# Performance work log

Measured on AMD Instinct MI355X. Metric: run time of the kernel, lower is better.

The kernel has to match this reference:

```python
import jax, jax.numpy as jnp
import numpy as np

K = 20  # n_neighbors
SLOPE = 0.2

def _act(h):
    return jax.nn.leaky_relu(h, negative_slope=SLOPE)

def _knn_indices(pts):
    # pts: (B, 3, N). Returns (B, N, K) indices of nearest neighbors (by -||xi-xj||^2).
    sq = jnp.sum(pts * pts, axis=1)                      # (B, N)
    inner = jnp.einsum('bcn,bcm->bnm', pts, pts)         # (B, N, N)
    neg_dist = 2.0 * inner - sq[:, :, None] - sq[:, None, :]
    _, idx = jax.lax.top_k(neg_dist, K)                  # (B, N, K)
    return idx

def _gather_neighbors(feats, idx):
    # feats: (B, N, C), idx: (B, N, K) -> (B, N, K, C)
    return jax.vmap(lambda f, i: f[i])(feats, idx)

def setup_inputs() -> dict:
    key = jax.random.key(0)
    ks = jax.random.split(key, 7)
    B, N = 16, 2048
    dims = [64, 64, 128, 256]
    s = 0.05
    inp = {
        'x':  jax.random.normal(ks[0], (B, N, 3), jnp.float32),
        'W0': jax.random.normal(ks[1], (dims[0], 6), jnp.float32) * s,
        'b0': jnp.zeros((dims[0],), jnp.float32),
        'W1': jax.random.normal(ks[2], (dims[1], dims[0]), jnp.float32) * s,
        'b1': jnp.zeros((dims[1],), jnp.float32),
        'W2': jax.random.normal(ks[3], (dims[2], dims[1]), jnp.float32) * s,
        'b2': jnp.zeros((dims[2],), jnp.float32),
        'W3': jax.random.normal(ks[4], (dims[3], dims[2]), jnp.float32) * s,
        'b3': jnp.zeros((dims[3],), jnp.float32),
        'Wf': jax.random.normal(ks[5], (1024, sum(dims)), jnp.float32) * s,
        'bf': jnp.zeros((1024,), jnp.float32),
    }
    return inp

def reference(x, W0, b0, W1, b1, W2, b2, W3, b3, Wf, bf):
    # x: (B, N, 3)
    pts = jnp.swapaxes(x, 1, 2)                          # (B, 3, N)
    idx = _knn_indices(pts)                              # (B, N, K)

    # get_graph_features: edge feats = [neighbor - center, center], (B, N, K, 6)
    neigh = _gather_neighbors(x, idx)                    # (B, N, K, 3)
    center = jnp.broadcast_to(x[:, :, None, :], neigh.shape)
    edge = jnp.concatenate([neigh - center, center], axis=-1)

    # EdgeConv (1x1 conv) + act, then max over neighbors
    h = _act(jnp.einsum('bnkc,oc->bnko', edge, W0) + b0)  # (B, N, K, 64)
    feat = jnp.max(h, axis=2)                             # (B, N, 64)

    xs = [feat]
    for W, b in ((W1, b1), (W2, b2), (W3, b3)):
        # graph max pooling over the fixed kNN graph
        pooled = jnp.max(_gather_neighbors(feat, idx), axis=2)  # (B, N, C)
        feat = _act(jnp.einsum('bnc,oc->bno', pooled, W) + b)
        xs.append(feat)

    cat = jnp.concatenate(xs, axis=-1)                    # (B, N, 512)
    out = _act(jnp.einsum('bnc,oc->bno', cat, Wf) + bf)   # (B, N, 1024)
    return jnp.max(out, axis=1)                           # (B, 1024)
```

## Files before the change

kernel.cpp:

```cpp
#include <hip/hip_runtime.h>

#define K_NN 20
#define NEG_INF (-__builtin_inff())

constexpr int BB   = 16;
constexpr int NN   = 2048;
constexpr int CATC = 512;
constexpr int ROW_G = BB * NN;

typedef short bf16x8 __attribute__((ext_vector_type(8)));
typedef float f32x4  __attribute__((ext_vector_type(4)));

__device__ __forceinline__ unsigned short f2bf_rn(float f) {
  unsigned int u = __float_as_uint(f);
  unsigned int r = u + 0x7FFFu + ((u >> 16) & 1u);
  return (unsigned short)(r >> 16);
}
__device__ __forceinline__ float bf2f(unsigned short h) {
  return __uint_as_float((unsigned int)h << 16);
}
__device__ __forceinline__ void split_store(float v, unsigned short* ph, unsigned short* pl) {
  const unsigned short h = f2bf_rn(v);
  *ph = h;
  *pl = f2bf_rn(v - bf2f(h));
}
__device__ __forceinline__ float join_hl(unsigned short h, unsigned short l) {
  return bf2f(h) + bf2f(l);
}

__device__ __forceinline__ int mbcnt(unsigned long long mask) {
  return __builtin_amdgcn_mbcnt_hi((unsigned int)(mask >> 32),
         __builtin_amdgcn_mbcnt_lo((unsigned int)mask, 0));
}

#define DECL_VALS(INIT) \
  unsigned int v0=INIT,v1=INIT,v2=INIT,v3=INIT,v4=INIT,v5=INIT,v6=INIT,v7=INIT, \
               v8=INIT,v9=INIT,v10=INIT,v11=INIT,v12=INIT,v13=INIT,v14=INIT,    \
               v15=INIT,v16=INIT,v17=INIT,v18=INIT,v19=INIT;

#define INSERT_VAL(x) do {                         \
    v19 = min(v18, max(v19, (x)));                 \
    v18 = min(v17, max(v18, (x)));                 \
    v17 = min(v16, max(v17, (x)));                 \
    v16 = min(v15, max(v16, (x)));                 \
    v15 = min(v14, max(v15, (x)));                 \
    v14 = min(v13, max(v14, (x)));                 \
    v13 = min(v12, max(v13, (x)));                 \
    v12 = min(v11, max(v12, (x)));                 \
    v11 = min(v10, max(v11, (x)));                 \
    v10 = min(v9,  max(v10, (x)));                 \
    v9  = min(v8,  max(v9,  (x)));                 \
    v8  = min(v7,  max(v8,  (x)));                 \
    v7  = min(v6,  max(v7,  (x)));                 \
    v6  = min(v5,  max(v6,  (x)));                 \
    v5  = min(v4,  max(v5,  (x)));                 \
    v4  = min(v3,  max(v4,  (x)));                 \
    v3  = min(v2,  max(v3,  (x)));                 \
    v2  = min(v1,  max(v2,  (x)));                 \
    v1  = min(v0,  max(v1,  (x)));                 \
    v0  = max(v0, (x));                            \
  } while (0)

__device__ __forceinline__ unsigned int sortable(float d) {
  unsigned int ub = __float_as_uint(d);
  return (ub & 0x80000000u) ? ~ub : (ub | 0x80000000u);
}

__global__ __launch_bounds__(128) void knn_chunk_kernel(const float* __restrict__ x,
                                                        unsigned int* __restrict__ cv) {
  __shared__ float4 cand[256];
  const int bid = blockIdx.x;
  const int ch = bid & 7;
  const int rt = (bid >> 3) & 15;
  const int b  = bid >> 7;
  const float* xb = x + (size_t)b * NN * 3;

  for (int i = threadIdx.x; i < 256; i += 128) {
    const int m = ch * 256 + i;
    const float px = xb[m*3+0], py = xb[m*3+1], pz = xb[m*3+2];
    cand[i] = make_float4(px, py, pz, fmaf(pz, pz, fmaf(py, py, px*px)));
  }
  __syncthreads();

  const int n = rt * 128 + threadIdx.x;
  const float cx = xb[n*3+0], cy = xb[n*3+1], cz = xb[n*3+2];
  const float csq = fmaf(cz, cz, fmaf(cy, cy, cx*cx));

  DECL_VALS(0u)

#pragma unroll 4
  for (int i = 0; i < 256; ++i) {
    const float4 c = cand[i];
    const float inner = fmaf(cz, c.z, fmaf(cy, c.y, cx*c.x));
    const float d = 2.0f * inner - csq - c.w;
    const unsigned int u = sortable(d);
    INSERT_VAL(u);
  }

  const int rowg = b * NN + n;
#define STORE_VAL(i) cv[(size_t)(ch*K_NN + i) * ROW_G + rowg] = v##i;
  STORE_VAL(0) STORE_VAL(1) STORE_VAL(2) STORE_VAL(3) STORE_VAL(4)
  STORE_VAL(5) STORE_VAL(6) STORE_VAL(7) STORE_VAL(8) STORE_VAL(9)
  STORE_VAL(10) STORE_VAL(11) STORE_VAL(12) STORE_VAL(13) STORE_VAL(14)
  STORE_VAL(15) STORE_VAL(16) STORE_VAL(17) STORE_VAL(18) STORE_VAL(19)
#undef STORE_VAL
}

__global__ __launch_bounds__(64) void knn_d20_kernel(const unsigned int* __restrict__ cv,
                                                     unsigned int* __restrict__ d20g) {
  const int r = blockIdx.x * 64 + threadIdx.x;
#define LOAD_VAL(i) unsigned int v##i = cv[(size_t)i * ROW_G + r];
  LOAD_VAL(0) LOAD_VAL(1) LOAD_VAL(2) LOAD_VAL(3) LOAD_VAL(4)
  LOAD_VAL(5) LOAD_VAL(6) LOAD_VAL(7) LOAD_VAL(8) LOAD_VAL(9)
  LOAD_VAL(10) LOAD_VAL(11) LOAD_VAL(12) LOAD_VAL(13) LOAD_VAL(14)
  LOAD_VAL(15) LOAD_VAL(16) LOAD_VAL(17) LOAD_VAL(18) LOAD_VAL(19)
#undef LOAD_VAL
#pragma unroll 4
  for (int i = K_NN; i < 8 * K_NN; ++i)
    INSERT_VAL(cv[(size_t)i * ROW_G + r]);
  d20g[r] = v19;
}

__global__ __launch_bounds__(256) void knn_collect_kernel(const float* __restrict__ x,
    const unsigned int* __restrict__ d20g, int* __restrict__ idx_out) {
  __shared__ float4 cand[NN];
  __shared__ int tie[4][K_NN];
  const int w = threadIdx.x >> 6, lane = threadIdx.x & 63;
  const int r = blockIdx.x * 4 + w;
  const int b = r >> 11;
  const float* xb = x + (size_t)b * NN * 3;

  for (int i = threadIdx.x; i < NN; i += 256) {
    const float px = xb[i*3+0], py = xb[i*3+1], pz = xb[i*3+2];
    cand[i] = make_float4(px, py, pz, fmaf(pz, pz, fmaf(py, py, px*px)));
  }
  __syncthreads();

  const int n = r & (NN - 1);
  const float4 ctr = cand[n];
  const unsigned int d20 = d20g[r];
  int* op = idx_out + (size_t)r * K_NN;
  int cg = 0, ce = 0;

#pragma unroll 4
  for (int k = 0; k < NN / 64; ++k) {
    const int i = k * 64 + lane;
    const float4 c = cand[i];
    const float inner = fmaf(ctr.z, c.z, fmaf(ctr.y, c.y, ctr.x*c.x));
    const float d = 2.0f * inner - ctr.w - c.w;
    const unsigned int u = sortable(d);
    const unsigned long long mb = __ballot(u > d20);
    if (u > d20) op[cg + mbcnt(mb)] = i;
    cg += __popcll(mb);
    const unsigned long long tb = __ballot(u == d20);
    if (tb) {
      if (u == d20) {
        const int pos = ce + mbcnt(tb);
        if (pos < K_NN) tie[w][pos] = i;
      }
      ce += __popcll(tb);
    }
  }
  if (lane == 0)
    for (int j = 0; cg < K_NN; ++j, ++cg) op[cg] = tie[w][j];
}

__global__ __launch_bounds__(256) void edgeconv_kernel(const float* __restrict__ x,
    const int* __restrict__ idx, const float* __restrict__ W0,
    const float* __restrict__ b0, unsigned short* __restrict__ Ahg,
    unsigned short* __restrict__ Alg) {
  const int o  = threadIdx.x & 63;
  const int pt = blockIdx.x * 4 + (threadIdx.x >> 6);
  const int b  = pt >> 11, n = pt & (NN - 1);
  const float* xb = x + (size_t)b * NN * 3;

  const float w0 = W0[o*6+0], w1 = W0[o*6+1], w2 = W0[o*6+2];
  const float w3 = W0[o*6+3], w4 = W0[o*6+4], w5 = W0[o*6+5];
  const float bias = b0[o];
  const float cx = xb[n*3+0], cy = xb[n*3+1], cz = xb[n*3+2];

  const int* ip = idx + (size_t)pt * K_NN;
  float px = 0.f, py = 0.f, pz = 0.f;
  if (o < K_NN) { const int m = ip[o]; px = xb[m*3+0]; py = xb[m*3+1]; pz = xb[m*3+2]; }

  float best = NEG_INF;
#pragma unroll
  for (int k = 0; k < K_NN; ++k) {
    const float ax = __shfl(px, k, 64), ay = __shfl(py, k, 64), az = __shfl(pz, k, 64);
    float h = w0 * (ax - cx);
    h = fmaf(w1, ay - cy, h);
    h = fmaf(w2, az - cz, h);
    h = fmaf(w3, cx, h);
    h = fmaf(w4, cy, h);
    h = fmaf(w5, cz, h);
    h += bias;
    h = (h > 0.f) ? h : 0.2f * h;
    best = fmaxf(best, h);
  }
  split_store(best, &Ahg[(size_t)pt * CATC + o], &Alg[(size_t)pt * CATC + o]);
}

template<int CIN, int COUT, int PTS>
__global__ __launch_bounds__(256) void pool_mlp_kernel(
    unsigned short* __restrict__ Ahg, unsigned short* __restrict__ Alg,
    const int* __restrict__ idx, const float* __restrict__ W,
    const float* __restrict__ bias, int coff_in, int coff_out) {
  __shared__ float pooled[PTS][CIN];
  __shared__ int sidx[PTS][K_NN];
  const int pt0 = blockIdx.x * PTS;

  for (int t = threadIdx.x; t < PTS * K_NN; t += 256)
    sidx[t / K_NN][t % K_NN] = idx[(size_t)pt0 * K_NN + t];
  __syncthreads();

  for (int t = threadIdx.x; t < PTS * CIN; t += 256) {
    const int p = t / CIN, c = t % CIN;
    const int bq = (pt0 + p) >> 11;
    const size_t base = (size_t)bq * NN * CATC + coff_in + c;
    float mv = NEG_INF;
#pragma unroll
    for (int k = 0; k < K_NN; ++k) {
      const size_t a = base + (size_t)sidx[p][k] * CATC;
      mv = fmaxf(mv, join_hl(Ahg[a], Alg[a]));
    }
    pooled[p][c] = mv;
  }
  __syncthreads();

  for (int t = threadIdx.x; t < PTS * COUT; t += 256) {
    const int p = t / COUT, o = t % COUT;
    const float4* pp = (const float4*)&pooled[p][0];
    const float4* wp = (const float4*)(W + (size_t)o * CIN);
    float acc = 0.f;
#pragma unroll
    for (int c4 = 0; c4 < CIN / 4; ++c4) {
      const float4 pv = pp[c4], wv = wp[c4];
      acc = fmaf(pv.x, wv.x, acc);
      acc = fmaf(pv.y, wv.y, acc);
      acc = fmaf(pv.z, wv.z, acc);
      acc = fmaf(pv.w, wv.w, acc);
    }
    float h = acc + bias[o];
    h = (h > 0.f) ? h : 0.2f * h;
    const size_t a = (size_t)(pt0 + p) * CATC + coff_out + o;
    split_store(h, &Ahg[a], &Alg[a]);
  }
}

__global__ __launch_bounds__(256) void wsplit_kernel(const float* __restrict__ Wf,
    unsigned short* __restrict__ Wh, unsigned short* __restrict__ Wl) {
  const int t = blockIdx.x * 256 + threadIdx.x;
  const float4 v = ((const float4*)Wf)[t];
  ushort4 h4, l4;
  h4.x = f2bf_rn(v.x); l4.x = f2bf_rn(v.x - bf2f(h4.x));
  h4.y = f2bf_rn(v.y); l4.y = f2bf_rn(v.y - bf2f(h4.y));
  h4.z = f2bf_rn(v.z); l4.z = f2bf_rn(v.z - bf2f(h4.z));
  h4.w = f2bf_rn(v.w); l4.w = f2bf_rn(v.w - bf2f(h4.w));
  ((ushort4*)Wh)[t] = h4;
  ((ushort4*)Wl)[t] = l4;
}

__global__ __launch_bounds__(256) void final_gemm_mfma(
    const unsigned short* __restrict__ Ahg, const unsigned short* __restrict__ Alg,
    const unsigned short* __restrict__ Whg, const unsigned short* __restrict__ Wlg,
    float* __restrict__ partials) {
  __shared__ __align__(16) unsigned short AhL[128][40];
  __shared__ __align__(16) unsigned short AlL[128][40];
  __shared__ __align__(16) unsigned short WhL[128][40];
  __shared__ __align__(16) unsigned short WlL[128][40];

  const int L     = blockIdx.x + (blockIdx.y << 3) + (blockIdx.z << 7);
  const int xcd   = L & 7;
  const int q     = L >> 3;
  const int ot    = q & 7;
  const int s     = q >> 3;
  const int p     = (s << 3) | xcd;
  const int chunk = p & 15;
  const int b     = p >> 4;

  const int tid   = threadIdx.x;
  const int lane  = tid & 63;
  const int w     = tid >> 6;
  const int wr    = w >> 1;
  const int wc    = w & 1;
  const int fr    = lane & 15;
  const int kg    = lane >> 4;

  const int srow = tid >> 1;
  const int shalf = (tid & 1) * 16;
  const size_t arow = ((size_t)(b * NN) + (size_t)chunk * 128 + srow) * CATC;
  const size_t wrow = ((size_t)ot * 128 + srow) * CATC;

  f32x4 acc[4][4];
#pragma unroll
  for (int i = 0; i < 4; ++i)
#pragma unroll
    for (int j = 0; j < 4; ++j) acc[i][j] = (f32x4){0.f, 0.f, 0.f, 0.f};

  uint4 ra0 = *(const uint4*)(Ahg + arow + shalf);
  uint4 ra1 = *(const uint4*)(Ahg + arow + shalf + 8);
  uint4 ra2 = *(const uint4*)(Alg + arow + shalf);
  uint4 ra3 = *(const uint4*)(Alg + arow + shalf + 8);
  uint4 rw0 = *(const uint4*)(Whg + wrow + shalf);
  uint4 rw1 = *(const uint4*)(Whg + wrow + shalf + 8);
  uint4 rw2 = *(const uint4*)(Wlg + wrow + shalf);
  uint4 rw3 = *(const uint4*)(Wlg + wrow + shalf + 8);

  for (int kt = 0; kt < 16; ++kt) {
    __syncthreads();
    *(uint4*)&AhL[srow][shalf]     = ra0;
    *(uint4*)&AhL[srow][shalf + 8] = ra1;
    *(uint4*)&AlL[srow][shalf]     = ra2;
    *(uint4*)&AlL[srow][shalf + 8] = ra3;
    *(uint4*)&WhL[srow][shalf]     = rw0;
    *(uint4*)&WhL[srow][shalf + 8] = rw1;
    *(uint4*)&WlL[srow][shalf]     = rw2;
    *(uint4*)&WlL[srow][shalf + 8] = rw3;
    if (kt < 15) {
      const int k0 = (kt + 1) * 32;
      ra0 = *(const uint4*)(Ahg + arow + k0 + shalf);
      ra1 = *(const uint4*)(Ahg + arow + k0 + shalf + 8);
      ra2 = *(const uint4*)(Alg + arow + k0 + shalf);
      ra3 = *(const uint4*)(Alg + arow + k0 + shalf + 8);
      rw0 = *(const uint4*)(Whg + wrow + k0 + shalf);
      rw1 = *(const uint4*)(Whg + wrow + k0 + shalf + 8);
      rw2 = *(const uint4*)(Wlg + wrow + k0 + shalf);
      rw3 = *(const uint4*)(Wlg + wrow + k0 + shalf + 8);
    }
    __syncthreads();

    bf16x8 ahf[4], alf[4], whf[4], wlf[4];
#pragma unroll
    for (int i = 0; i < 4; ++i) {
      ahf[i] = *(const bf16x8*)&AhL[wr * 64 + i * 16 + fr][kg * 8];
      alf[i] = *(const bf16x8*)&AlL[wr * 64 + i * 16 + fr][kg * 8];
    }
#pragma unroll
    for (int j = 0; j < 4; ++j) {
      whf[j] = *(const bf16x8*)&WhL[wc * 64 + j * 16 + fr][kg * 8];
      wlf[j] = *(const bf16x8*)&WlL[wc * 64 + j * 16 + fr][kg * 8];
    }

#pragma unroll
    for (int i = 0; i < 4; ++i)
#pragma unroll
      for (int j = 0; j < 4; ++j) {
        acc[i][j] = __builtin_amdgcn_mfma_f32_16x16x32_bf16(ahf[i], whf[j], acc[i][j], 0, 0, 0);
        acc[i][j] = __builtin_amdgcn_mfma_f32_16x16x32_bf16(ahf[i], wlf[j], acc[i][j], 0, 0, 0);
        acc[i][j] = __builtin_amdgcn_mfma_f32_16x16x32_bf16(alf[i], whf[j], acc[i][j], 0, 0, 0);
      }
  }

  __syncthreads();
  float* smax = (float*)&AhL[0][0];
#pragma unroll
  for (int j = 0; j < 4; ++j) {
    float mj = NEG_INF;
#pragma unroll
    for (int i = 0; i < 4; ++i) {
      mj = fmaxf(mj, fmaxf(fmaxf(acc[i][j][0], acc[i][j][1]),
                           fmaxf(acc[i][j][2], acc[i][j][3])));
    }
    mj = fmaxf(mj, __shfl_xor(mj, 16, 64));
    mj = fmaxf(mj, __shfl_xor(mj, 32, 64));
    if (lane < 16) smax[wr * 128 + wc * 64 + j * 16 + fr] = mj;
  }
  __syncthreads();
  if (tid < 128) {
    const float m = fmaxf(smax[tid], smax[128 + tid]);
    partials[((size_t)(b * 16 + chunk)) * 1024 + (size_t)ot * 128 + tid] = m;
  }
}

__global__ __launch_bounds__(256) void final_reduce_kernel(const float* __restrict__ partials,
    const float* __restrict__ bf, float* __restrict__ out) {
  const int t = blockIdx.x * 256 + threadIdx.x;
  const int b = t >> 10, o = t & 1023;
  float m = NEG_INF;
#pragma unroll
  for (int c = 0; c < 16; ++c)
    m = fmaxf(m, partials[((size_t)(b * 16 + c)) * 1024 + o]);
  float h = m + bf[o];
  out[t] = (h > 0.f) ? h : 0.2f * h;
}

extern "C" void kernel_launch(void* const* d_in, const int* in_sizes, int n_in,
                              void* d_out, int out_size, void* d_ws, size_t ws_size,
                              hipStream_t stream) {
  (void)in_sizes; (void)n_in; (void)out_size; (void)ws_size;
  const float* x  = (const float*)d_in[0];
  const float* W0 = (const float*)d_in[1];
  const float* b0 = (const float*)d_in[2];
  const float* W1 = (const float*)d_in[3];
  const float* b1 = (const float*)d_in[4];
  const float* W2 = (const float*)d_in[5];
  const float* b2 = (const float*)d_in[6];
  const float* W3 = (const float*)d_in[7];
  const float* b3 = (const float*)d_in[8];
  const float* Wf = (const float*)d_in[9];
  const float* bf = (const float*)d_in[10];
  float* out = (float*)d_out;

  char* ws = (char*)d_ws;
  int* idx_ws = (int*)ws;
  unsigned short* Wh = (unsigned short*)ws;
  unsigned short* Wl = (unsigned short*)(ws + 1048576);
  unsigned int* cv = (unsigned int*)(ws + 2621440);
  unsigned int* d20g = (unsigned int*)(ws + 23592960);
  unsigned short* Ah = (unsigned short*)(ws + 2621440);
  unsigned short* Al = (unsigned short*)(ws + 36175872);
  float* partials = (float*)(ws + 69730304);

  knn_chunk_kernel<<<BB * 16 * 8, 128, 0, stream>>>(x, cv);
  knn_d20_kernel<<<ROW_G / 64, 64, 0, stream>>>(cv, d20g);
  knn_collect_kernel<<<ROW_G / 4, 256, 0, stream>>>(x, d20g, idx_ws);
  edgeconv_kernel<<<ROW_G / 4, 256, 0, stream>>>(x, idx_ws, W0, b0, Ah, Al);
  pool_mlp_kernel<64, 64, 16><<<ROW_G / 16, 256, 0, stream>>>(Ah, Al, idx_ws, W1, b1, 0, 64);
  pool_mlp_kernel<64, 128, 8><<<ROW_G / 8, 256, 0, stream>>>(Ah, Al, idx_ws, W2, b2, 64, 128);
  pool_mlp_kernel<128, 256, 8><<<ROW_G / 8, 256, 0, stream>>>(Ah, Al, idx_ws, W3, b3, 128, 256);
  wsplit_kernel<<<512, 256, 0, stream>>>(Wf, Wh, Wl);
  final_gemm_mfma<<<dim3(8, 16, BB), 256, 0, stream>>>(Ah, Al, Wh, Wl, partials);
  final_reduce_kernel<<<BB * 1024 / 256, 256, 0, stream>>>(partials, bf, out);
}
```

Baseline: 517.3 us.

## Vectorize neighbor gather and remap pool blocks for XCD-local batches

Each thread in the graph max-pooling stage now gathers 8 consecutive channels per neighbor with 16-byte loads of the hi and lo bf16 planes, replacing the old one-channel scalar gathers. Block indices are remapped so that each XCD handles two whole batches, which keeps neighbor gathers within one L2 slice. Points per block are also raised and the shared pooled array is padded. The trade-off is fewer active threads during the gather phase (some threads sit idle when PTS*CG < 256) and more work per block.

```diff
diff --git a/kernel.cpp b/kernel.cpp
--- a/kernel.cpp
+++ b/kernel.cpp
@@ -205,25 +205,48 @@
     unsigned short* __restrict__ Ahg, unsigned short* __restrict__ Alg,
     const int* __restrict__ idx, const float* __restrict__ W,
     const float* __restrict__ bias, int coff_in, int coff_out) {
-  __shared__ float pooled[PTS][CIN];
+  __shared__ float pooled[PTS][CIN + 4];
   __shared__ int sidx[PTS][K_NN];
-  const int pt0 = blockIdx.x * PTS;
+
+  constexpr int BPB = NN / PTS;
+  const int bid  = blockIdx.x;
+  const int xcd  = bid & 7;
+  const int s    = bid >> 3;
+  const int b    = xcd * 2 + s / BPB;
+  const int inner= s % BPB;
+  const int pt0  = b * NN + inner * PTS;
 
   for (int t = threadIdx.x; t < PTS * K_NN; t += 256)
     sidx[t / K_NN][t % K_NN] = idx[(size_t)pt0 * K_NN + t];
   __syncthreads();
 
-  for (int t = threadIdx.x; t < PTS * CIN; t += 256) {
-    const int p = t / CIN, c = t % CIN;
-    const int bq = (pt0 + p) >> 11;
-    const size_t base = (size_t)bq * NN * CATC + coff_in + c;
-    float mv = NEG_INF;
-#pragma unroll
-    for (int k = 0; k < K_NN; ++k) {
-      const size_t a = base + (size_t)sidx[p][k] * CATC;
-      mv = fmaxf(mv, join_hl(Ahg[a], Alg[a]));
-    }
-    pooled[p][c] = mv;
+  constexpr int CG = CIN / 8;
+  {
+    const int p  = threadIdx.x / CG;
+    const int c8 = threadIdx.x % CG;
+    if (p < PTS) {
+      const size_t base = (size_t)b * NN * CATC + coff_in + c8 * 8;
+      float mv[8];
+#pragma unroll
+      for (int j = 0; j < 8; ++j) mv[j] = NEG_INF;
+#pragma unroll 4
+      for (int k = 0; k < K_NN; ++k) {
+        const size_t a = base + (size_t)sidx[p][k] * CATC;
+        const uint4 h = *(const uint4*)(Ahg + a);
+        const uint4 l = *(const uint4*)(Alg + a);
+        const unsigned int hw[4] = {h.x, h.y, h.z, h.w};
+        const unsigned int lw[4] = {l.x, l.y, l.z, l.w};
+#pragma unroll
+        for (int q = 0; q < 4; ++q) {
+          const float f0 = __uint_as_float(hw[q] << 16) + __uint_as_float(lw[q] << 16);
+          const float f1 = __uint_as_float(hw[q] & 0xFFFF0000u) + __uint_as_float(lw[q] & 0xFFFF0000u);
+          mv[2*q+0] = fmaxf(mv[2*q+0], f0);
+          mv[2*q+1] = fmaxf(mv[2*q+1], f1);
+        }
+      }
+      *(float4*)&pooled[p][c8 * 8]     = make_float4(mv[0], mv[1], mv[2], mv[3]);
+      *(float4*)&pooled[p][c8 * 8 + 4] = make_float4(mv[4], mv[5], mv[6], mv[7]);
+    }
   }
   __syncthreads();
 
@@ -415,9 +438,9 @@
   knn_d20_kernel<<<ROW_G / 64, 64, 0, stream>>>(cv, d20g);
   knn_collect_kernel<<<ROW_G / 4, 256, 0, stream>>>(x, d20g, idx_ws);
   edgeconv_kernel<<<ROW_G / 4, 256, 0, stream>>>(x, idx_ws, W0, b0, Ah, Al);
-  pool_mlp_kernel<64, 64, 16><<<ROW_G / 16, 256, 0, stream>>>(Ah, Al, idx_ws, W1, b1, 0, 64);
-  pool_mlp_kernel<64, 128, 8><<<ROW_G / 8, 256, 0, stream>>>(Ah, Al, idx_ws, W2, b2, 64, 128);
-  pool_mlp_kernel<128, 256, 8><<<ROW_G / 8, 256, 0, stream>>>(Ah, Al, idx_ws, W3, b3, 128, 256);
+  pool_mlp_kernel<64, 64, 32><<<BB * (NN / 32), 256, 0, stream>>>(Ah, Al, idx_ws, W1, b1, 0, 64);
+  pool_mlp_kernel<64, 128, 32><<<BB * (NN / 32), 256, 0, stream>>>(Ah, Al, idx_ws, W2, b2, 64, 128);
+  pool_mlp_kernel<128, 256, 16><<<BB * (NN / 16), 256, 0, stream>>>(Ah, Al, idx_ws, W3, b3, 128, 256);
   wsplit_kernel<<<512, 256, 0, stream>>>(Wf, Wh, Wl);
   final_gemm_mfma<<<dim3(8, 16, BB), 256, 0, stream>>>(Ah, Al, Wh, Wl, partials);
   final_reduce_kernel<<<BB * 1024 / 256, 256, 0, stream>>>(partials, bf, out);
```

Result: slower. 559.8 us (+8.2%).
